# Kernel tuning notes

Hardware: AMD Instinct MI355X
Metric: run time of the kernel (lower is better)

## Reference

```python
import jax, jax.numpy as jnp
import numpy as np

N, C_IN, C_OUT, L, V, P, K, STRIDE = 8, 256, 256, 512, 25, 3, 9, 1
BN_EPS = 1e-5


def setup_inputs() -> dict:
    key = jax.random.key(0)
    k1, k2, k3, k4, k5 = jax.random.split(key, 5)
    x = jax.random.normal(k1, (N, C_IN, L, V), dtype=jnp.float32)
    # 1x1 Conv2d weight, no bias: (out_channels*num_partitions, in_channels)
    conv_w = jax.random.normal(k2, (C_OUT * P, C_IN), dtype=jnp.float32) * (1.0 / np.sqrt(C_IN))
    # adjacency (P, V, V)
    A = jax.random.normal(k3, (P, V, V), dtype=jnp.float32) * 0.2
    bn_gamma = jnp.ones((C_OUT,), dtype=jnp.float32)
    bn_beta = jnp.zeros((C_OUT,), dtype=jnp.float32)
    bn_mean = jax.random.normal(k4, (C_OUT,), dtype=jnp.float32) * 0.1
    bn_var = jax.random.uniform(k5, (C_OUT,), dtype=jnp.float32) + 0.5
    return {"x": x, "conv_w": conv_w, "A": A, "bn_gamma": bn_gamma,
            "bn_beta": bn_beta, "bn_mean": bn_mean, "bn_var": bn_var}


def reference(x, conv_w, A, bn_gamma, bn_beta, bn_mean, bn_var):
    # residual branch: identity (in_channels == out_channels, stride == 1)
    res = x
    # 1x1 conv: (N, C_in, L, V) -> (N, C_out*P, L, V)
    y = jnp.einsum('nclv,oc->nolv', x, conv_w)
    # split channels into P partitions, stack, permute -> (N, L, P, C_out, V)
    y = y.reshape(N, P, C_OUT, L, V).transpose(0, 3, 1, 2, 4)
    # graph aggregation: x @ A per partition
    y = jnp.einsum('nlpcv,pvw->nlpcw', y, A)
    # sum over partitions -> (N, L, C_out, V)
    s = y.sum(axis=2)
    # FIFO with zero init + strided taps == causal strided window sum:
    # out[t] = sum_{k=0}^{K-1} s[t - k*STRIDE], zero-padded for t-k*STRIDE < 0
    pad = (K - 1) * STRIDE
    s_pad = jnp.pad(s, ((0, 0), (pad, 0), (0, 0), (0, 0)))
    out = s_pad[:, 0:L]
    for k in range(1, K):
        out = out + s_pad[:, k * STRIDE:k * STRIDE + L]
    # stack along dim 2 in torch -> (N, C_out, L, V)
    out = out.transpose(0, 2, 1, 3)
    # BatchNorm2d (eval, running stats) + ReLU
    scale = bn_gamma * jax.lax.rsqrt(bn_var + BN_EPS)
    shift = bn_beta - bn_mean * scale
    out = out * scale[None, :, None, None] + shift[None, :, None, None]
    out = jax.nn.relu(out)
    # residual add, then ReLU (Dropout p=0.0 is identity)
    out = jax.nn.relu(out + res)
    return out
```

## Files before the change

kernel.cpp:

```cpp
#include <hip/hip_runtime.h>
#include <hip/hip_bf16.h>

#define NB 8
#define CC 256
#define OO 768
#define LL 512
#define VV 25
#define PP 3
#define KM 768
#define NKC 24
#define LT 4

typedef __attribute__((ext_vector_type(8))) short short8v;
typedef __attribute__((ext_vector_type(4))) float float4v;
typedef __attribute__((ext_vector_type(4))) int int4v;

__device__ inline short bf16b(float a){ __hip_bfloat16 h = __float2bfloat16(a); return *(short*)&h; }
__device__ inline unsigned pk2(float a, float b){
    __hip_bfloat16 ha = __float2bfloat16(a), hb = __float2bfloat16(b);
    unsigned short ua = *(unsigned short*)&ha, ub = *(unsigned short*)&hb;
    return (unsigned)ua | ((unsigned)ub << 16);
}
__device__ inline void gload_lds16(const void* g, void* s) {
    __builtin_amdgcn_global_load_lds((const __attribute__((address_space(1))) unsigned*)g,
                                     (__attribute__((address_space(3))) unsigned*)(s), 16, 0, 0);
}

__global__ __launch_bounds__(256) void wperm_kernel(const float* __restrict__ W,
                                                    __hip_bfloat16* __restrict__ Wp) {
    int idx = blockIdx.x * 256 + threadIdx.x;
    if (idx >= OO * CC) return;
    int c = idx / KM;
    int k = idx - c * KM;
    int cib = k / 192, r = k - cib * 192;
    int p = r >> 6, ci6 = r & 63;
    Wp[idx] = __float2bfloat16(W[(p * 256 + c) * 256 + cib * 64 + ci6]);
}

__global__ __launch_bounds__(512, 4) void fused_main_kernel(
    const float* __restrict__ x,
    const __hip_bfloat16* __restrict__ Wp,
    const float* __restrict__ A,
    const float* __restrict__ gamma, const float* __restrict__ beta,
    const float* __restrict__ mean, const float* __restrict__ var,
    float* __restrict__ out)
{
    __shared__ __hip_bfloat16 Wb[2][256 * 32];
    __shared__ __hip_bfloat16 Zb[2][128 * 32];
    __shared__ __hip_bfloat16 xsh[256 * 32];
    __shared__ __hip_bfloat16 a2t[3 * 32 * 32];
    __shared__ float scsh[512];

    const int tid  = threadIdx.x;
    const int lane = tid & 63, wid = tid >> 6;
    const int lcol = lane & 15, grp = lane >> 4;
    const int bid0 = blockIdx.x;
    const int swz = (bid0 & 7) * 128 + (bid0 >> 3);
    const int n  = swz >> 7;
    const int l0 = (swz & 127) * LT;
    const int wm = wid >> 1, wn = wid & 1;
    const int l_z = wid >> 1, mt_z = wid & 1;

    const int c_st  = tid >> 2;
    const int kb_st = (tid & 3) ^ ((c_st >> 1) & 3);

    {
        int4v z = {0, 0, 0, 0};
        ((int4v*)xsh)[tid] = z;
        ((int4v*)xsh)[tid + 512] = z;
        if (tid < 384) ((int4v*)a2t)[tid] = z;
        int c = tid & 255;
        float sc = gamma[c] * rsqrtf(var[c] + 1e-5f);
        if (tid < 256) scsh[tid] = sc;
        else           scsh[tid] = beta[c] - mean[c] * sc;
    }
    __syncthreads();
    for (int idx = tid; idx < PP * VV * VV; idx += 512) {
        int p = idx / 625, r = idx - p * 625, v = r / 25, w = r - v * 25;
        int R = p * 32 + w;
        int e = (((v >> 3) ^ ((R >> 1) & 3)) << 3) | (v & 7);
        a2t[R * 32 + e] = __float2bfloat16(A[idx]);
    }

    auto stage_w = [&](int buf, int kc_) {
        #pragma unroll
        for (int it = 0; it < 2; ++it) {
            const __hip_bfloat16* s = Wp + (size_t)(c_st + it * 128) * KM + kc_ * 32 + kb_st * 8;
            gload_lds16((const void*)s, (void*)((char*)&Wb[buf][0] + it * 8192 + wid * 1024));
        }
    };
    auto stage_xs = [&](int cib) {
        for (int cc = tid; cc < 1600; cc += 512) {
            int ci6 = cc / 25, v = cc - ci6 * 25;
            const float* xp = x + ((size_t)(n * CC + cib * 64 + ci6) * LL) * VV + v;
            float rbuf[12];
            #pragma unroll
            for (int j = 0; j < 12; ++j) {
                int lj = l0 - 8 + j;
                rbuf[j] = (lj >= 0) ? xp[(size_t)lj * VV] : 0.f;
            }
            float wsv = 0.f;
            #pragma unroll
            for (int j = 0; j < 9; ++j) wsv += rbuf[j];
            #pragma unroll
            for (int i = 0; i < 4; ++i) {
                int R = ci6 * 4 + i;
                int e = (((v >> 3) ^ ((R >> 2) & 3)) << 3) | (v & 7);
                xsh[R * 32 + e] = __float2bfloat16(wsv);
                if (i < 3) wsv += rbuf[9 + i] - rbuf[i];
            }
        }
    };
    auto zgen = [&](int kc, int zbuf) {
        int p = (kc % 6) >> 1, h = kc & 1;
        int ci6 = h * 32 + mt_z * 16 + lcol;
        int R = ci6 * 4 + l_z;
        short8v az = *(const short8v*)&xsh[R * 32 + ((grp ^ ((R >> 2) & 3)) << 3)];
        #pragma unroll
        for (int wt = 0; wt < 2; ++wt) {
            int R2 = p * 32 + wt * 16 + lcol;
            short8v bz = *(const short8v*)&a2t[R2 * 32 + ((grp ^ ((R2 >> 1) & 3)) << 3)];
            float4v zc = {0.f, 0.f, 0.f, 0.f};
            zc = __builtin_amdgcn_mfma_f32_16x16x32_bf16(az, bz, zc, 0, 0, 0);
            int R3 = l_z * 32 + wt * 16 + lcol;
            int eb = (mt_z * 2 + (grp >> 1)) ^ ((R3 >> 1) & 3);
            unsigned* dst = (unsigned*)&Zb[zbuf][R3 * 32 + (eb << 3) + ((grp & 1) << 2)];
            dst[0] = pk2(zc[0], zc[1]);
            dst[1] = pk2(zc[2], zc[3]);
        }
    };

    float4v acc[4][4];
    #pragma unroll
    for (int i = 0; i < 4; ++i)
        #pragma unroll
        for (int j = 0; j < 4; ++j) acc[i][j] = (float4v){0.f, 0.f, 0.f, 0.f};

    stage_w(0, 0);

    #pragma unroll 1
    for (int cib = 0; cib < 4; ++cib) {
        stage_xs(cib);
        asm volatile("s_waitcnt lgkmcnt(0)" ::: "memory");
        __builtin_amdgcn_sched_barrier(0);
        __builtin_amdgcn_s_barrier();
        __builtin_amdgcn_sched_barrier(0);

        zgen(cib * 6, (cib * 6) & 1);
        asm volatile("s_waitcnt lgkmcnt(0) vmcnt(0)" ::: "memory");
        __builtin_amdgcn_sched_barrier(0);
        __builtin_amdgcn_s_barrier();
        __builtin_amdgcn_sched_barrier(0);

        #pragma unroll 1
        for (int j = 0; j < 6; ++j) {
            const int kc = cib * 6 + j;
            if (kc + 1 < NKC) stage_w((kc + 1) & 1, kc + 1);

            if (j < 5) zgen(kc + 1, (kc + 1) & 1);

            const __hip_bfloat16* wcur = &Wb[kc & 1][0];
            const __hip_bfloat16* zcur = &Zb[kc & 1][0];
            short8v af[4], bf[4];
            #pragma unroll
            for (int mt = 0; mt < 4; ++mt) {
                int c = wm * 64 + mt * 16 + lcol;
                af[mt] = *(const short8v*)&wcur[c * 32 + ((grp ^ ((c >> 1) & 3)) << 3)];
            }
            #pragma unroll
            for (int nt = 0; nt < 4; ++nt) {
                int R3 = wn * 64 + nt * 16 + lcol;
                bf[nt] = *(const short8v*)&zcur[R3 * 32 + ((grp ^ ((R3 >> 1) & 3)) << 3)];
            }

            __builtin_amdgcn_s_setprio(1);
            #pragma unroll
            for (int mt = 0; mt < 4; ++mt)
                #pragma unroll
                for (int nt = 0; nt < 4; ++nt)
                    acc[mt][nt] = __builtin_amdgcn_mfma_f32_16x16x32_bf16(af[mt], bf[nt], acc[mt][nt], 0, 0, 0);
            __builtin_amdgcn_s_setprio(0);

            asm volatile("s_waitcnt lgkmcnt(0)" ::: "memory");
            __builtin_amdgcn_sched_barrier(0);
            if (kc + 1 < NKC) { asm volatile("s_waitcnt vmcnt(2)" ::: "memory"); }
            else              { asm volatile("s_waitcnt vmcnt(0)" ::: "memory"); }
            __builtin_amdgcn_sched_barrier(0);
            __builtin_amdgcn_s_barrier();
            __builtin_amdgcn_sched_barrier(0);
        }
    }

    #pragma unroll
    for (int mt = 0; mt < 4; ++mt) {
        #pragma unroll
        for (int nt = 0; nt < 4; ++nt) {
            int w = (wn * 64 + nt * 16) & 31;
            int l = l0 + ((wn * 64 + nt * 16) >> 5);
            int wl = w + lcol;
            if (wl < VV) {
                #pragma unroll
                for (int r = 0; r < 4; ++r) {
                    int c = wm * 64 + mt * 16 + grp * 4 + r;
                    float val = fmaf(acc[mt][nt][r], scsh[c], scsh[256 + c]);
                    val = fmaxf(val, 0.f);
                    size_t ad = ((size_t)(n * CC + c) * LL + l) * VV + wl;
                    val = fmaxf(val + x[ad], 0.f);
                    out[ad] = val;
                }
            }
        }
    }
}

__global__ __launch_bounds__(256) void wsum_kernel(const float* __restrict__ x,
                                                   float* __restrict__ xs) {
    const int CHUNKS = 8;
    int t = blockIdx.x * 256 + threadIdx.x;
    if (t >= NB * CC * VV * CHUNKS) return;
    int v = t % VV;
    int r = t / VV;
    int chunk = r % CHUNKS;
    int nc = r / CHUNKS;
    int l0 = chunk * (LL / CHUNKS);
    const float* xp = x  + (size_t)nc * (LL * VV) + v;
    float*       op = xs + (size_t)nc * (LL * VV) + v;
    float ring[8];
    float run = 0.f;
    #pragma unroll
    for (int k = 0; k < 8; ++k) {
        int j = l0 - 8 + k;
        float val = (j >= 0) ? xp[j * VV] : 0.f;
        ring[k] = val; run += val;
    }
    for (int base = l0; base < l0 + LL / CHUNKS; base += 8) {
        #pragma unroll
        for (int k = 0; k < 8; ++k) {
            int l = base + k;
            float val = xp[l * VV];
            float o = run + val;
            op[l * VV] = o;
            run = o - ring[k];
            ring[k] = val;
        }
    }
}

__global__ __launch_bounds__(256) void fused_fallback_kernel(
    const float* xs, const float* __restrict__ x, const float* __restrict__ W,
    const float* __restrict__ A,
    const float* __restrict__ gamma, const float* __restrict__ beta,
    const float* __restrict__ mean, const float* __restrict__ var,
    float* out)
{
    __shared__ float xshf[CC][28];
    const int bid = blockIdx.x;
    const int n = bid >> 9;
    const int l = bid & 511;
    const int tid = threadIdx.x;
    const size_t nbase = (size_t)n * CC * LL * VV;
    for (int k = tid; k < CC * VV; k += 256) {
        int ci = k / VV, v = k - ci * VV;
        xshf[ci][v] = xs[nbase + (size_t)ci * (LL * VV) + (size_t)l * VV + v];
    }
    __syncthreads();
    const int c = tid;
    float Y[PP * VV];
    #pragma unroll
    for (int i = 0; i < PP * VV; ++i) Y[i] = 0.f;
    const float* Wpr = W + c * 256;
    #pragma unroll 1
    for (int ci = 0; ci < CC; ++ci) {
        float xv[VV];
        #pragma unroll
        for (int v = 0; v < VV; ++v) xv[v] = xshf[ci][v];
        float w0 = Wpr[ci], w1 = Wpr[65536 + ci], w2 = Wpr[131072 + ci];
        #pragma unroll
        for (int v = 0; v < VV; ++v) Y[v]          = fmaf(w0, xv[v], Y[v]);
        #pragma unroll
        for (int v = 0; v < VV; ++v) Y[VV + v]     = fmaf(w1, xv[v], Y[VV + v]);
        #pragma unroll
        for (int v = 0; v < VV; ++v) Y[2 * VV + v] = fmaf(w2, xv[v], Y[2 * VV + v]);
    }
    float o[VV];
    #pragma unroll
    for (int w = 0; w < VV; ++w) o[w] = 0.f;
    #pragma unroll
    for (int p = 0; p < PP; ++p)
        #pragma unroll
        for (int v = 0; v < VV; ++v) {
            float y = Y[p * VV + v];
            const float* Ap = A + (p * VV + v) * VV;
            #pragma unroll
            for (int w = 0; w < VV; ++w) o[w] = fmaf(y, Ap[w], o[w]);
        }
    float sc = gamma[c] * rsqrtf(var[c] + 1e-5f);
    float sh = beta[c] - mean[c] * sc;
    const float* resp = x   + nbase + (size_t)c * (LL * VV) + (size_t)l * VV;
    float*       outp = out + nbase + (size_t)c * (LL * VV) + (size_t)l * VV;
    #pragma unroll
    for (int w = 0; w < VV; ++w) {
        float t2 = fmaf(o[w], sc, sh);
        t2 = fmaxf(t2, 0.f);
        t2 = fmaxf(t2 + resp[w], 0.f);
        outp[w] = t2;
    }
}

extern "C" void kernel_launch(void* const* d_in, const int* in_sizes, int n_in,
                              void* d_out, int out_size, void* d_ws, size_t ws_size,
                              hipStream_t stream) {
    const float* x  = (const float*)d_in[0];
    const float* W  = (const float*)d_in[1];
    const float* A  = (const float*)d_in[2];
    const float* gm = (const float*)d_in[3];
    const float* bt = (const float*)d_in[4];
    const float* mn = (const float*)d_in[5];
    const float* vr = (const float*)d_in[6];
    float* out = (float*)d_out;

    if (ws_size >= (size_t)(OO * CC * sizeof(__hip_bfloat16))) {
        __hip_bfloat16* Wp = (__hip_bfloat16*)d_ws;
        wperm_kernel<<<dim3((OO * CC + 255) / 256), dim3(256), 0, stream>>>(W, Wp);
        fused_main_kernel<<<dim3(NB * (LL / LT)), dim3(512), 0, stream>>>(
            x, Wp, A, gm, bt, mn, vr, out);
    } else {
        const int threadsA = NB * CC * VV * 8;
        wsum_kernel<<<dim3((threadsA + 255) / 256), dim3(256), 0, stream>>>(x, out);
        fused_fallback_kernel<<<dim3(NB * LL), dim3(256), 0, stream>>>(
            out, x, W, A, gm, bt, mn, vr, out);
    }
}
```

Before: 112.7 us.

## Load weight MFMA fragments directly from global memory in fragment-ordered layout

The weight permutation kernel now stores bf16 weights in MFMA-fragment order (kc, wm, mt, lane, 8 elements), so each lane can read its A fragment with one contiguous 16-byte global load. The double-buffered LDS staging of weights and its vmcnt waits are removed, which frees LDS and cuts LDS traffic and synchronization. The cost is that each block re-reads weights through L2/global with load latency exposed inside the k-loop, now covered only by the zgen work issued between the load and the MFMAs.

```diff
diff --git a/kernel.cpp b/kernel.cpp
--- a/kernel.cpp
+++ b/kernel.cpp
@@ -15,26 +15,28 @@
 typedef __attribute__((ext_vector_type(4))) float float4v;
 typedef __attribute__((ext_vector_type(4))) int int4v;
 
-__device__ inline short bf16b(float a){ __hip_bfloat16 h = __float2bfloat16(a); return *(short*)&h; }
 __device__ inline unsigned pk2(float a, float b){
     __hip_bfloat16 ha = __float2bfloat16(a), hb = __float2bfloat16(b);
     unsigned short ua = *(unsigned short*)&ha, ub = *(unsigned short*)&hb;
     return (unsigned)ua | ((unsigned)ub << 16);
 }
-__device__ inline void gload_lds16(const void* g, void* s) {
-    __builtin_amdgcn_global_load_lds((const __attribute__((address_space(1))) unsigned*)g,
-                                     (__attribute__((address_space(3))) unsigned*)(s), 16, 0, 0);
-}
 
 __global__ __launch_bounds__(256) void wperm_kernel(const float* __restrict__ W,
                                                     __hip_bfloat16* __restrict__ Wp) {
     int idx = blockIdx.x * 256 + threadIdx.x;
     if (idx >= OO * CC) return;
-    int c = idx / KM;
-    int k = idx - c * KM;
-    int cib = k / 192, r = k - cib * 192;
-    int p = r >> 6, ci6 = r & 63;
-    Wp[idx] = __float2bfloat16(W[(p * 256 + c) * 256 + cib * 64 + ci6]);
+    int j    = idx & 7;
+    int lane = (idx >> 3) & 63;
+    int mt   = (idx >> 9) & 3;
+    int wm   = (idx >> 11) & 3;
+    int kc   = idx >> 13;
+    int c = wm * 64 + mt * 16 + (lane & 15);
+    int k = kc * 32 + ((lane >> 4) << 3) + j;
+    int cib = k / 192;
+    int r = k - cib * 192;
+    int p = r >> 6;
+    int ci = cib * 64 + (r & 63);
+    Wp[idx] = __float2bfloat16(W[(p * 256 + c) * 256 + ci]);
 }
 
 __global__ __launch_bounds__(512, 4) void fused_main_kernel(
@@ -45,7 +47,6 @@
     const float* __restrict__ mean, const float* __restrict__ var,
     float* __restrict__ out)
 {
-    __shared__ __hip_bfloat16 Wb[2][256 * 32];
     __shared__ __hip_bfloat16 Zb[2][128 * 32];
     __shared__ __hip_bfloat16 xsh[256 * 32];
     __shared__ __hip_bfloat16 a2t[3 * 32 * 32];
@@ -61,9 +62,6 @@
     const int wm = wid >> 1, wn = wid & 1;
     const int l_z = wid >> 1, mt_z = wid & 1;
 
-    const int c_st  = tid >> 2;
-    const int kb_st = (tid & 3) ^ ((c_st >> 1) & 3);
-
     {
         int4v z = {0, 0, 0, 0};
         ((int4v*)xsh)[tid] = z;
@@ -82,13 +80,6 @@
         a2t[R * 32 + e] = __float2bfloat16(A[idx]);
     }
 
-    auto stage_w = [&](int buf, int kc_) {
-        #pragma unroll
-        for (int it = 0; it < 2; ++it) {
-            const __hip_bfloat16* s = Wp + (size_t)(c_st + it * 128) * KM + kc_ * 32 + kb_st * 8;
-            gload_lds16((const void*)s, (void*)((char*)&Wb[buf][0] + it * 8192 + wid * 1024));
-        }
-    };
     auto stage_xs = [&](int cib) {
         for (int cc = tid; cc < 1600; cc += 512) {
             int ci6 = cc / 25, v = cc - ci6 * 25;
@@ -136,7 +127,7 @@
         #pragma unroll
         for (int j = 0; j < 4; ++j) acc[i][j] = (float4v){0.f, 0.f, 0.f, 0.f};
 
-    stage_w(0, 0);
+    const __hip_bfloat16* afbase = Wp + ((size_t)(wm * 4) * 64 + lane) * 8;
 
     #pragma unroll 1
     for (int cib = 0; cib < 4; ++cib) {
@@ -147,7 +138,7 @@
         __builtin_amdgcn_sched_barrier(0);
 
         zgen(cib * 6, (cib * 6) & 1);
-        asm volatile("s_waitcnt lgkmcnt(0) vmcnt(0)" ::: "memory");
+        asm volatile("s_waitcnt lgkmcnt(0)" ::: "memory");
         __builtin_amdgcn_sched_barrier(0);
         __builtin_amdgcn_s_barrier();
         __builtin_amdgcn_sched_barrier(0);
@@ -155,18 +146,19 @@
         #pragma unroll 1
         for (int j = 0; j < 6; ++j) {
             const int kc = cib * 6 + j;
-            if (kc + 1 < NKC) stage_w((kc + 1) & 1, kc + 1);
+
+            short8v af[4];
+            {
+                const __hip_bfloat16* ap = afbase + kc * 8192;
+                #pragma unroll
+                for (int mt = 0; mt < 4; ++mt)
+                    af[mt] = *(const short8v*)(ap + mt * 512);
+            }
 
             if (j < 5) zgen(kc + 1, (kc + 1) & 1);
 
-            const __hip_bfloat16* wcur = &Wb[kc & 1][0];
             const __hip_bfloat16* zcur = &Zb[kc & 1][0];
-            short8v af[4], bf[4];
-            #pragma unroll
-            for (int mt = 0; mt < 4; ++mt) {
-                int c = wm * 64 + mt * 16 + lcol;
-                af[mt] = *(const short8v*)&wcur[c * 32 + ((grp ^ ((c >> 1) & 3)) << 3)];
-            }
+            short8v bf[4];
             #pragma unroll
             for (int nt = 0; nt < 4; ++nt) {
                 int R3 = wn * 64 + nt * 16 + lcol;
@@ -182,9 +174,6 @@
             __builtin_amdgcn_s_setprio(0);
 
             asm volatile("s_waitcnt lgkmcnt(0)" ::: "memory");
-            __builtin_amdgcn_sched_barrier(0);
-            if (kc + 1 < NKC) { asm volatile("s_waitcnt vmcnt(2)" ::: "memory"); }
-            else              { asm volatile("s_waitcnt vmcnt(0)" ::: "memory"); }
             __builtin_amdgcn_sched_barrier(0);
             __builtin_amdgcn_s_barrier();
             __builtin_amdgcn_sched_barrier(0);
```

Result: faster. 107.3 us (-4.7%).
